# Performance work log

Measured on AMD Instinct MI355X. Metric: run time of the kernel, lower is better.

Reference implementation:

```python
import jax, jax.numpy as jnp
import numpy as np

N, E, G = 10000, 160000, 64
F, C1, C2, C3, K, NC = 128, 128, 256, 512, 5, 10


def setup_inputs() -> dict:
    key = jax.random.key(0)
    ks = jax.random.split(key, 12)
    s = 0.05
    return {
        "x": jax.random.normal(ks[0], (N, F), dtype=jnp.float32),
        "edge_index": jax.random.randint(ks[1], (2, E), 0, N, dtype=jnp.int64),
        "batch": jnp.sort(jax.random.randint(ks[2], (N,), 0, G, dtype=jnp.int64)),
        "W_cheb": jax.random.normal(ks[3], (K, F, C1), dtype=jnp.float32) * s,
        "b_cheb": jnp.zeros((C1,), jnp.float32),
        "W_g1": jax.random.normal(ks[4], (C1, C2), dtype=jnp.float32) * s,
        "b_g1": jnp.zeros((C2,), jnp.float32),
        "W_g2": jax.random.normal(ks[5], (C2, C3), dtype=jnp.float32) * s,
        "b_g2": jnp.zeros((C3,), jnp.float32),
        "w_gate": jax.random.normal(ks[6], (C3, 1), dtype=jnp.float32) * s,
        "b_gate": jnp.zeros((1,), jnp.float32),
        "W_fc": jax.random.normal(ks[7], (C3, NC), dtype=jnp.float32) * s,
        "b_fc": jnp.zeros((NC,), jnp.float32),
    }


def _deg_inv_sqrt(deg):
    return jnp.where(deg > 0, jax.lax.rsqrt(jnp.maximum(deg, 1e-12)), 0.0)


def cheb_conv(x, src, dst, W, b):
    # PyG ChebConv, sym normalization, lambda_max=2 => scaled Laplacian = -D^-1/2 A D^-1/2
    ones = jnp.ones((src.shape[0],), x.dtype)
    deg = jax.ops.segment_sum(ones, src, num_segments=N)
    dinv = _deg_inv_sqrt(deg)
    w = -(dinv[src] * dinv[dst])  # [E]

    def prop(h):
        return jax.ops.segment_sum(w[:, None] * h[src], dst, num_segments=N)

    tx0 = x
    tx1 = prop(x)
    out = tx0 @ W[0] + tx1 @ W[1]
    for k in range(2, W.shape[0]):
        tx2 = 2.0 * prop(tx1) - tx0
        out = out + tx2 @ W[k]
        tx0, tx1 = tx1, tx2
    return out + b


def gcn_conv(x, src, dst, W, b):
    # PyG GCNConv: add self-loops, sym norm D~^-1/2 (A+I) D~^-1/2, transform then aggregate
    loop = jnp.arange(N, dtype=src.dtype)
    src_a = jnp.concatenate([src, loop])
    dst_a = jnp.concatenate([dst, loop])
    ones = jnp.ones((src_a.shape[0],), x.dtype)
    deg = jax.ops.segment_sum(ones, dst_a, num_segments=N)
    dinv = _deg_inv_sqrt(deg)
    norm = dinv[src_a] * dinv[dst_a]  # [E+N]
    h = x @ W
    return jax.ops.segment_sum(norm[:, None] * h[src_a], dst_a, num_segments=N) + b


def attention_pool(x, batch, w_gate, b_gate):
    logits = (x @ w_gate + b_gate)[:, 0]  # [N]
    m = jax.ops.segment_max(logits, batch, num_segments=G)
    e = jnp.exp(logits - m[batch])
    s = jax.ops.segment_sum(e, batch, num_segments=G)
    alpha = e / s[batch]
    return jax.ops.segment_sum(alpha[:, None] * x, batch, num_segments=G)  # [G, C3]


def reference(x, edge_index, batch, W_cheb, b_cheb, W_g1, b_g1, W_g2, b_g2,
              w_gate, b_gate, W_fc, b_fc):
    src, dst = edge_index[0], edge_index[1]
    h = jax.nn.relu(cheb_conv(x, src, dst, W_cheb, b_cheb))
    h = jax.nn.relu(gcn_conv(h, src, dst, W_g1, b_g1))
    h = jax.nn.relu(gcn_conv(h, src, dst, W_g2, b_g2))
    g = attention_pool(h, batch, w_gate, b_gate)
    logits = g @ W_fc + b_fc
    return jax.nn.log_softmax(logits, axis=1)
```

## Files before the change

kernel.cpp:

```cpp
#include <hip/hip_runtime.h>
#include <hip/hip_bf16.h>
#include <math.h>

#define N_NODES 10000
#define N_EDGES 160000
#define N_GRAPHS 64
#define F_IN    128
#define C1_DIM  128
#define C2_DIM  256
#define C3_DIM  512
#define K_CHEB  5
#define NCLS    10
#define TC      (K_CHEB * F_IN)

typedef short v8s __attribute__((ext_vector_type(8)));
typedef float v4f __attribute__((ext_vector_type(4)));

static __device__ __forceinline__ unsigned short f2bf(float f) {
    unsigned u = __float_as_uint(f);
    unsigned r = (u + 0x7FFFu + ((u >> 16) & 1u)) >> 16;
    return (unsigned short)r;
}
static __device__ __forceinline__ float bf_lo(unsigned u) { return __uint_as_float(u << 16); }
static __device__ __forceinline__ float bf_hi(unsigned u) { return __uint_as_float(u & 0xFFFF0000u); }

#define PREP_A (N_NODES * 64)
#define PREP_B (TC * C1_DIM)
#define PREP_C (C1_DIM * C2_DIM)
#define PREP_D (C2_DIM * C3_DIM)
#define PREP_E N_NODES
#define PREP_F N_NODES
#define PREP_G N_EDGES
#define PREP_TOTAL (PREP_A + PREP_B + PREP_C + PREP_D + PREP_E + PREP_F + PREP_G)
__global__ void prep_kernel(const float* __restrict__ x, unsigned short* __restrict__ tcat,
                            const float* __restrict__ Wcheb, unsigned short* __restrict__ Wcb_t,
                            const float* __restrict__ Wg1, unsigned short* __restrict__ Wg1_t,
                            const float* __restrict__ Wg2, unsigned short* __restrict__ Wg2_t,
                            const int* __restrict__ batch, int* __restrict__ gptr,
                            float* __restrict__ logits,
                            const int* __restrict__ src, const int* __restrict__ dst,
                            int* __restrict__ cnt_s, int* __restrict__ cnt_d) {
    int id = blockIdx.x * blockDim.x + threadIdx.x;
    if (id < PREP_A) {
        int n = id >> 6, f = (id & 63) * 2;
        float2 v = *(const float2*)(x + (size_t)n * F_IN + f);
        ushort2 o; o.x = f2bf(v.x); o.y = f2bf(v.y);
        *(ushort2*)(tcat + (size_t)n * TC + f) = o;
        return;
    }
    id -= PREP_A;
    if (id < PREP_B) {
        int n = id % C1_DIM, k = id / C1_DIM;
        Wcb_t[(size_t)n * TC + k] = f2bf(Wcheb[(size_t)k * C1_DIM + n]);
        return;
    }
    id -= PREP_B;
    if (id < PREP_C) {
        int n = id % C2_DIM, k = id / C2_DIM;
        Wg1_t[(size_t)n * C1_DIM + k] = f2bf(Wg1[(size_t)k * C2_DIM + n]);
        return;
    }
    id -= PREP_C;
    if (id < PREP_D) {
        int n = id % C3_DIM, k = id / C3_DIM;
        Wg2_t[(size_t)n * C2_DIM + k] = f2bf(Wg2[(size_t)k * C3_DIM + n]);
        return;
    }
    id -= PREP_D;
    if (id < PREP_E) {
        int i = id;
        int b = batch[i];
        if (i == 0) { for (int g = 0; g <= b; g++) gptr[g] = 0; }
        else {
            int bp = batch[i - 1];
            for (int g = bp + 1; g <= b; g++) gptr[g] = i;
        }
        if (i == N_NODES - 1) { for (int g = b + 1; g <= N_GRAPHS; g++) gptr[g] = N_NODES; }
        return;
    }
    id -= PREP_E;
    if (id < PREP_F) { logits[id] = 0.0f; return; }
    id -= PREP_F;
    if (id < PREP_G) {
        atomicAdd(&cnt_s[src[id]], 1);
        atomicAdd(&cnt_d[dst[id]], 1);
    }
}

__global__ __launch_bounds__(256) void scan_kernel(const int* __restrict__ cnt_d,
                                                   int* __restrict__ rowptr, int n) {
    __shared__ int ldsc[N_NODES];
    __shared__ int sums[256];
    int tid = threadIdx.x;
    for (int i = tid; i < n; i += 256) ldsc[i] = cnt_d[i];
    __syncthreads();
    int chunk = (n + 255) / 256;
    int s0 = tid * chunk, s1 = min(n, s0 + chunk);
    if (s0 > n) s0 = n;
    int loc = 0;
    for (int i = s0; i < s1; i++) loc += ldsc[i];
    sums[tid] = loc;
    __syncthreads();
    for (int off = 1; off < 256; off <<= 1) {
        int t = (tid >= off) ? sums[tid - off] : 0;
        __syncthreads();
        sums[tid] += t;
        __syncthreads();
    }
    int pre = sums[tid] - loc;
    for (int i = s0; i < s1; i++) { int v = ldsc[i]; ldsc[i] = pre; pre += v; }
    __syncthreads();
    for (int i = tid; i < n; i += 256) rowptr[i] = ldsc[i];
    if (tid == 255) rowptr[n] = pre;
}

__global__ void fill_kernel(const int* __restrict__ src, const int* __restrict__ dst,
                            const int* __restrict__ cnt_s, const int* __restrict__ cnt_d,
                            const int* __restrict__ rowptr, int* __restrict__ fillc,
                            int* __restrict__ col, float* __restrict__ wch,
                            float* __restrict__ nrm, int E) {
    int e = blockIdx.x * blockDim.x + threadIdx.x;
    if (e >= E) return;
    int s = src[e], d = dst[e];
    int pos = rowptr[d] + atomicAdd(&fillc[d], 1);
    col[pos] = s;
    int cs = cnt_s[s], cd = cnt_s[d];
    float ds = (cs > 0) ? rsqrtf((float)cs) : 0.0f;
    float dd = (cd > 0) ? rsqrtf((float)cd) : 0.0f;
    wch[pos] = -(ds * dd);
    nrm[pos] = rsqrtf((float)cnt_d[s] + 1.0f) * rsqrtf((float)cnt_d[d] + 1.0f);
}

__global__ __launch_bounds__(256) void gather_cheb_bf(
        const unsigned short* __restrict__ tb, const int* __restrict__ rowptr,
        const int* __restrict__ col, const float* __restrict__ ew,
        const unsigned short* __restrict__ base, float alpha, float beta,
        unsigned short* __restrict__ outc, int n) {
    int w = (blockIdx.x * blockDim.x + threadIdx.x) >> 6;
    int lane = threadIdx.x & 63;
    if (w >= n) return;
    float a0 = 0.0f, a1 = 0.0f;
    int rs = rowptr[w], re = rowptr[w + 1];
    for (int b = rs; b < re; b += 64) {
        int cl = 0; float wl = 0.0f;
        if (b + lane < re) { cl = col[b + lane]; wl = ew[b + lane]; }
        int nk8 = (min(64, re - b) + 7) & ~7;
        for (int j = 0; j < nk8; j += 8) {
            int ss[8]; float ww[8]; unsigned uu[8];
            #pragma unroll
            for (int q = 0; q < 8; q++) { ss[q] = __shfl(cl, j + q); ww[q] = __shfl(wl, j + q); }
            #pragma unroll
            for (int q = 0; q < 8; q++) uu[q] = ((const unsigned*)(tb + (size_t)ss[q] * TC))[lane];
            #pragma unroll
            for (int q = 0; q < 8; q++) { a0 += ww[q] * bf_lo(uu[q]); a1 += ww[q] * bf_hi(uu[q]); }
        }
    }
    if (base) {
        unsigned ub = ((const unsigned*)(base + (size_t)w * TC))[lane];
        a0 = alpha * a0 + beta * bf_lo(ub);
        a1 = alpha * a1 + beta * bf_hi(ub);
    } else {
        a0 *= alpha; a1 *= alpha;
    }
    ushort2 o; o.x = f2bf(a0); o.y = f2bf(a1);
    *(ushort2*)(outc + (size_t)w * TC + lane * 2) = o;
}

template<int FPL>
__global__ __launch_bounds__(256) void gather_gcn_pre(
        const unsigned short* __restrict__ tb, const int* __restrict__ rowptr,
        const int* __restrict__ col, const float* __restrict__ ew,
        const int* __restrict__ cnt_d, unsigned short* __restrict__ z, int n) {
    const int C = FPL * 64;
    int w = (blockIdx.x * blockDim.x + threadIdx.x) >> 6;
    int lane = threadIdx.x & 63;
    if (w >= n) return;
    float acc[FPL];
    #pragma unroll
    for (int q = 0; q < FPL; q++) acc[q] = 0.0f;
    int rs = rowptr[w], re = rowptr[w + 1];
    for (int b = rs; b < re; b += 64) {
        int cl = 0; float wl = 0.0f;
        if (b + lane < re) { cl = col[b + lane]; wl = ew[b + lane]; }
        int nk8 = (min(64, re - b) + 7) & ~7;
        for (int j = 0; j < nk8; j += 8) {
            int ss[8]; float ww[8];
            #pragma unroll
            for (int q = 0; q < 8; q++) { ss[q] = __shfl(cl, j + q); ww[q] = __shfl(wl, j + q); }
            if constexpr (FPL == 2) {
                unsigned uu[8];
                #pragma unroll
                for (int q = 0; q < 8; q++) uu[q] = ((const unsigned*)(tb + (size_t)ss[q] * C))[lane];
                #pragma unroll
                for (int q = 0; q < 8; q++) {
                    acc[0] += ww[q] * bf_lo(uu[q]);
                    acc[1] += ww[q] * bf_hi(uu[q]);
                }
            } else {
                uint2 uu[8];
                #pragma unroll
                for (int q = 0; q < 8; q++) uu[q] = ((const uint2*)(tb + (size_t)ss[q] * C))[lane];
                #pragma unroll
                for (int q = 0; q < 8; q++) {
                    acc[0] += ww[q] * bf_lo(uu[q].x); acc[1] += ww[q] * bf_hi(uu[q].x);
                    acc[2] += ww[q] * bf_lo(uu[q].y); acc[3] += ww[q] * bf_hi(uu[q].y);
                }
            }
        }
    }
    float sn = 1.0f / (float)(cnt_d[w] + 1);
    if constexpr (FPL == 2) {
        unsigned u = ((const unsigned*)(tb + (size_t)w * C))[lane];
        acc[0] += sn * bf_lo(u); acc[1] += sn * bf_hi(u);
        ushort2 o; o.x = f2bf(acc[0]); o.y = f2bf(acc[1]);
        *(ushort2*)(z + (size_t)w * C + lane * 2) = o;
    } else {
        uint2 u = ((const uint2*)(tb + (size_t)w * C))[lane];
        acc[0] += sn * bf_lo(u.x); acc[1] += sn * bf_hi(u.x);
        acc[2] += sn * bf_lo(u.y); acc[3] += sn * bf_hi(u.y);
        ushort4 o; o.x = f2bf(acc[0]); o.y = f2bf(acc[1]);
        o.z = f2bf(acc[2]); o.w = f2bf(acc[3]);
        *(ushort4*)(z + (size_t)w * C + lane * 4) = o;
    }
}

template<int JT>
__global__ __launch_bounds__(256) void gemm_bf16(
        const unsigned short* __restrict__ A, const unsigned short* __restrict__ Bt,
        const float* __restrict__ bias, float* __restrict__ Cf,
        unsigned short* __restrict__ Cb, const float* __restrict__ wg,
        float* __restrict__ logits, int M, int K, int N, int relu) {
    int m0 = blockIdx.y * 64, n0 = blockIdx.x * (JT * 32);
    int wave = threadIdx.x >> 6, lane = threadIdx.x & 63;
    int wm = (wave & 1) * 32, wn = (wave >> 1) * (JT * 16);
    int l15 = lane & 15, quad = lane >> 4;

    v4f acc[2][JT];
    #pragma unroll
    for (int i = 0; i < 2; i++)
        #pragma unroll
        for (int j = 0; j < JT; j++) acc[i][j] = (v4f){0.f, 0.f, 0.f, 0.f};

    const unsigned short* Ab[2]; bool av[2];
    #pragma unroll
    for (int i = 0; i < 2; i++) {
        int row = m0 + wm + i * 16 + l15;
        av[i] = row < M;
        Ab[i] = A + (size_t)(av[i] ? row : 0) * K + quad * 8;
    }
    const unsigned short* Bb[JT];
    #pragma unroll
    for (int j = 0; j < JT; j++) {
        int coln = n0 + wn + j * 16 + l15;
        Bb[j] = Bt + (size_t)coln * K + quad * 8;
    }
    const v8s zero8 = {0, 0, 0, 0, 0, 0, 0, 0};

    for (int k0 = 0; k0 < K; k0 += 32) {
        v8s a[2], b[JT];
        #pragma unroll
        for (int i = 0; i < 2; i++) a[i] = av[i] ? *(const v8s*)(Ab[i] + k0) : zero8;
        #pragma unroll
        for (int j = 0; j < JT; j++) b[j] = *(const v8s*)(Bb[j] + k0);
        #pragma unroll
        for (int i = 0; i < 2; i++)
            #pragma unroll
            for (int j = 0; j < JT; j++)
                acc[i][j] = __builtin_amdgcn_mfma_f32_16x16x32_bf16(a[i], b[j], acc[i][j], 0, 0, 0);
    }

    float bv[JT], wgj[JT];
    #pragma unroll
    for (int j = 0; j < JT; j++) {
        int coln = n0 + wn + j * 16 + l15;
        bv[j] = bias[coln];
        wgj[j] = wg ? wg[coln] : 0.0f;
    }
    #pragma unroll
    for (int i = 0; i < 2; i++) {
        #pragma unroll
        for (int r = 0; r < 4; r++) {
            int row = m0 + wm + i * 16 + quad * 4 + r;
            if (row >= M) continue;
            float gval = 0.0f;
            #pragma unroll
            for (int j = 0; j < JT; j++) {
                int coln = n0 + wn + j * 16 + l15;
                float v = acc[i][j][r] + bv[j];
                if (relu) v = fmaxf(v, 0.0f);
                if (Cf) Cf[(size_t)row * N + coln] = v;
                else    Cb[(size_t)row * N + coln] = f2bf(v);
                gval += v * wgj[j];
            }
            if (wg) {
                #pragma unroll
                for (int off = 1; off < 16; off <<= 1) gval += __shfl_xor(gval, off);
                if (l15 == 0) atomicAdd(&logits[row], gval);
            }
        }
    }
}

__global__ __launch_bounds__(256) void pool_stats(float* __restrict__ logits,
                                                  const int* __restrict__ gptr,
                                                  float* __restrict__ pooled) {
    __shared__ float red[256];
    int g = blockIdx.x, tid = threadIdx.x;
    int gs = gptr[g], ge = gptr[g + 1];
    pooled[(size_t)g * C3_DIM + tid] = 0.0f;
    pooled[(size_t)g * C3_DIM + 256 + tid] = 0.0f;
    float m = -INFINITY;
    for (int i = gs + tid; i < ge; i += 256) m = fmaxf(m, logits[i]);
    red[tid] = m; __syncthreads();
    for (int off = 128; off > 0; off >>= 1) {
        if (tid < off) red[tid] = fmaxf(red[tid], red[tid + off]);
        __syncthreads();
    }
    m = red[0]; __syncthreads();
    float s = 0.0f;
    for (int i = gs + tid; i < ge; i += 256) s += expf(logits[i] - m);
    red[tid] = s; __syncthreads();
    for (int off = 128; off > 0; off >>= 1) {
        if (tid < off) red[tid] += red[tid + off];
        __syncthreads();
    }
    s = red[0];
    float sinv = (s > 0.0f) ? 1.0f / s : 0.0f;
    for (int i = gs + tid; i < ge; i += 256)
        logits[i] = expf(logits[i] - m) * sinv;
}

__global__ __launch_bounds__(256) void pool_partial(const unsigned short* __restrict__ h3b,
        const float* __restrict__ alpha, const int* __restrict__ gptr,
        float* __restrict__ pooled) {
    int g = blockIdx.x, sl = blockIdx.y, tid = threadIdx.x;
    int gs = gptr[g], ge = gptr[g + 1];
    int cnt = ge - gs;
    int i0 = gs + (cnt * sl) / 8;
    int i1 = gs + (cnt * (sl + 1)) / 8;
    float a0 = 0.0f, a1 = 0.0f;
    for (int i = i0; i < i1; i++) {
        float al = alpha[i];
        unsigned u = ((const unsigned*)(h3b + (size_t)i * C3_DIM))[tid];
        a0 += al * bf_lo(u);
        a1 += al * bf_hi(u);
    }
    if (i1 > i0) {
        atomicAdd(&pooled[(size_t)g * C3_DIM + tid * 2 + 0], a0);
        atomicAdd(&pooled[(size_t)g * C3_DIM + tid * 2 + 1], a1);
    }
}

__global__ void fc_kernel(const float* __restrict__ pooled, const float* __restrict__ Wfc,
                          const float* __restrict__ bfc, float* __restrict__ out) {
    int g = blockIdx.x;
    int t = threadIdx.x;
    float acc = -INFINITY;
    if (t < NCLS) {
        acc = bfc[t];
        for (int k = 0; k < C3_DIM; k++)
            acc += pooled[(size_t)g * C3_DIM + k] * Wfc[k * NCLS + t];
    }
    float m = acc;
    #pragma unroll
    for (int off = 8; off > 0; off >>= 1) m = fmaxf(m, __shfl_xor(m, off, 16));
    float e = (t < NCLS) ? expf(acc - m) : 0.0f;
    float s = e;
    #pragma unroll
    for (int off = 8; off > 0; off >>= 1) s += __shfl_xor(s, off, 16);
    if (t < NCLS) out[g * NCLS + t] = acc - m - logf(s);
}

extern "C" void kernel_launch(void* const* d_in, const int* in_sizes, int n_in,
                              void* d_out, int out_size, void* d_ws, size_t ws_size,
                              hipStream_t stream) {
    const float* x      = (const float*)d_in[0];
    const int*   ei     = (const int*)d_in[1];
    const int*   batch  = (const int*)d_in[2];
    const float* W_cheb = (const float*)d_in[3];
    const float* b_cheb = (const float*)d_in[4];
    const float* W_g1   = (const float*)d_in[5];
    const float* b_g1   = (const float*)d_in[6];
    const float* W_g2   = (const float*)d_in[7];
    const float* b_g2   = (const float*)d_in[8];
    const float* w_gate = (const float*)d_in[9];
    const float* W_fc   = (const float*)d_in[11];
    const float* b_fc   = (const float*)d_in[12];
    const int* src = ei;
    const int* dst = ei + N_EDGES;
    float* out = (float*)d_out;

    const int N = N_NODES, E = N_EDGES, G = N_GRAPHS;

    char* Wp = (char*)d_ws;
    auto alloc = [&](size_t bytes) {
        void* p = Wp;
        Wp += (bytes + 255) & ~(size_t)255;
        return p;
    };
    int*   cnt3    = (int*)alloc((size_t)3 * N * 4);
    int*   cnt_s   = cnt3;
    int*   cnt_d   = cnt3 + N;
    int*   fillc   = cnt3 + 2 * N;
    int*   rowptr  = (int*)alloc((N + 1) * 4);
    int*   col     = (int*)alloc(E * 4);
    float* wch     = (float*)alloc(E * 4);
    float* nrm     = (float*)alloc(E * 4);
    unsigned short* tcat  = (unsigned short*)alloc((size_t)N * TC * 2);
    unsigned short* h1b   = (unsigned short*)alloc((size_t)N * C1_DIM * 2);
    unsigned short* z1b   = (unsigned short*)alloc((size_t)N * C1_DIM * 2);
    unsigned short* h2b   = (unsigned short*)alloc((size_t)N * C2_DIM * 2);
    unsigned short* z2b   = (unsigned short*)alloc((size_t)N * C2_DIM * 2);
    unsigned short* h3b   = (unsigned short*)alloc((size_t)N * C3_DIM * 2);
    unsigned short* Wcb_t = (unsigned short*)alloc((size_t)TC * C1_DIM * 2);
    unsigned short* Wg1_t = (unsigned short*)alloc((size_t)C1_DIM * C2_DIM * 2);
    unsigned short* Wg2_t = (unsigned short*)alloc((size_t)C2_DIM * C3_DIM * 2);
    float* logits  = (float*)alloc(N * 4);
    int*   gptr    = (int*)alloc((G + 1) * 4);
    float* pooled  = (float*)alloc((size_t)G * C3_DIM * 4);

    dim3 blk(256);
    auto cdiv = [](int a, int b) { return (a + b - 1) / b; };

    hipMemsetAsync(cnt3, 0, (size_t)3 * N * sizeof(int), stream);
    hipLaunchKernelGGL(prep_kernel, dim3(cdiv(PREP_TOTAL, 256)), blk, 0, stream,
                       x, tcat, W_cheb, Wcb_t, W_g1, Wg1_t, W_g2, Wg2_t,
                       batch, gptr, logits, src, dst, cnt_s, cnt_d);

    hipLaunchKernelGGL(scan_kernel, dim3(1), blk, 0, stream, cnt_d, rowptr, N);
    hipLaunchKernelGGL(fill_kernel, dim3(cdiv(E, 256)), blk, 0, stream,
                       src, dst, cnt_s, cnt_d, rowptr, fillc, col, wch, nrm, E);

    const int NWB = cdiv(N, 4);

    hipLaunchKernelGGL(gather_cheb_bf, dim3(NWB), blk, 0, stream,
                       tcat + 0 * F_IN, rowptr, col, wch,
                       (const unsigned short*)nullptr, 1.0f, 0.0f, tcat + 1 * F_IN, N);
    hipLaunchKernelGGL(gather_cheb_bf, dim3(NWB), blk, 0, stream,
                       tcat + 1 * F_IN, rowptr, col, wch,
                       tcat + 0 * F_IN, 2.0f, -1.0f, tcat + 2 * F_IN, N);
    hipLaunchKernelGGL(gather_cheb_bf, dim3(NWB), blk, 0, stream,
                       tcat + 2 * F_IN, rowptr, col, wch,
                       tcat + 1 * F_IN, 2.0f, -1.0f, tcat + 3 * F_IN, N);
    hipLaunchKernelGGL(gather_cheb_bf, dim3(NWB), blk, 0, stream,
                       tcat + 3 * F_IN, rowptr, col, wch,
                       tcat + 2 * F_IN, 2.0f, -1.0f, tcat + 4 * F_IN, N);

    hipLaunchKernelGGL(gemm_bf16<2>, dim3(C1_DIM / 64, cdiv(N, 64)), blk, 0, stream,
                       tcat, Wcb_t, b_cheb, (float*)nullptr, h1b,
                       (const float*)nullptr, (float*)nullptr, N, TC, C1_DIM, 1);

    hipLaunchKernelGGL(gather_gcn_pre<2>, dim3(NWB), blk, 0, stream,
                       h1b, rowptr, col, nrm, cnt_d, z1b, N);
    hipLaunchKernelGGL(gemm_bf16<4>, dim3(C2_DIM / 128, cdiv(N, 64)), blk, 0, stream,
                       z1b, Wg1_t, b_g1, (float*)nullptr, h2b,
                       (const float*)nullptr, (float*)nullptr, N, C1_DIM, C2_DIM, 1);

    hipLaunchKernelGGL(gather_gcn_pre<4>, dim3(NWB), blk, 0, stream,
                       h2b, rowptr, col, nrm, cnt_d, z2b, N);
    hipLaunchKernelGGL(gemm_bf16<4>, dim3(C3_DIM / 128, cdiv(N, 64)), blk, 0, stream,
                       z2b, Wg2_t, b_g2, (float*)nullptr, h3b,
                       w_gate, logits, N, C2_DIM, C3_DIM, 1);

    hipLaunchKernelGGL(pool_stats, dim3(G), blk, 0, stream, logits, gptr, pooled);
    hipLaunchKernelGGL(pool_partial, dim3(G, 8), blk, 0, stream, h3b, logits, gptr, pooled);

    hipLaunchKernelGGL(fc_kernel, dim3(G), dim3(64), 0, stream, pooled, W_fc, b_fc, out);
}
```

Measured before the change: 265.4 us.

## Pack edge index and weight into int2, fuse pool stats, coalesce weight prep

Edge columns and weights are interleaved into int2 arrays, one for the Chebyshev weights and one for the GCN norms, so each gather kernel reads a single 8-byte load per edge instead of two separate arrays. The pool_stats kernel is merged into pool_partial: each block recomputes the per-graph max and sum and applies the softmax weight inline, and zeroing of the pooled buffer moves into prep_kernel. The weight-transpose loops in prep now index so consecutive threads write consecutive output elements. This saves a kernel launch and some memory traffic, at the cost of recomputing the segment statistics in all 8 slices of each graph.

After: 263.8 us. About the same (-0.6%).

```diff
diff --git a/kernel.cpp b/kernel.cpp
--- a/kernel.cpp
+++ b/kernel.cpp
@@ -30,14 +30,15 @@
 #define PREP_D (C2_DIM * C3_DIM)
 #define PREP_E N_NODES
 #define PREP_F N_NODES
+#define PREP_H (N_GRAPHS * C3_DIM)
 #define PREP_G N_EDGES
-#define PREP_TOTAL (PREP_A + PREP_B + PREP_C + PREP_D + PREP_E + PREP_F + PREP_G)
+#define PREP_TOTAL (PREP_A + PREP_B + PREP_C + PREP_D + PREP_E + PREP_F + PREP_H + PREP_G)
 __global__ void prep_kernel(const float* __restrict__ x, unsigned short* __restrict__ tcat,
                             const float* __restrict__ Wcheb, unsigned short* __restrict__ Wcb_t,
                             const float* __restrict__ Wg1, unsigned short* __restrict__ Wg1_t,
                             const float* __restrict__ Wg2, unsigned short* __restrict__ Wg2_t,
                             const int* __restrict__ batch, int* __restrict__ gptr,
-                            float* __restrict__ logits,
+                            float* __restrict__ logits, float* __restrict__ pooled,
                             const int* __restrict__ src, const int* __restrict__ dst,
                             int* __restrict__ cnt_s, int* __restrict__ cnt_d) {
     int id = blockIdx.x * blockDim.x + threadIdx.x;
@@ -50,19 +51,19 @@
     }
     id -= PREP_A;
     if (id < PREP_B) {
-        int n = id % C1_DIM, k = id / C1_DIM;
+        int k = id % TC, n = id / TC;
         Wcb_t[(size_t)n * TC + k] = f2bf(Wcheb[(size_t)k * C1_DIM + n]);
         return;
     }
     id -= PREP_B;
     if (id < PREP_C) {
-        int n = id % C2_DIM, k = id / C2_DIM;
+        int k = id % C1_DIM, n = id / C1_DIM;
         Wg1_t[(size_t)n * C1_DIM + k] = f2bf(Wg1[(size_t)k * C2_DIM + n]);
         return;
     }
     id -= PREP_C;
     if (id < PREP_D) {
-        int n = id % C3_DIM, k = id / C3_DIM;
+        int k = id % C2_DIM, n = id / C2_DIM;
         Wg2_t[(size_t)n * C2_DIM + k] = f2bf(Wg2[(size_t)k * C3_DIM + n]);
         return;
     }
@@ -81,6 +82,8 @@
     id -= PREP_E;
     if (id < PREP_F) { logits[id] = 0.0f; return; }
     id -= PREP_F;
+    if (id < PREP_H) { pooled[id] = 0.0f; return; }
+    id -= PREP_H;
     if (id < PREP_G) {
         atomicAdd(&cnt_s[src[id]], 1);
         atomicAdd(&cnt_d[dst[id]], 1);
@@ -117,23 +120,22 @@
 __global__ void fill_kernel(const int* __restrict__ src, const int* __restrict__ dst,
                             const int* __restrict__ cnt_s, const int* __restrict__ cnt_d,
                             const int* __restrict__ rowptr, int* __restrict__ fillc,
-                            int* __restrict__ col, float* __restrict__ wch,
-                            float* __restrict__ nrm, int E) {
+                            int2* __restrict__ ecb, int2* __restrict__ egc, int E) {
     int e = blockIdx.x * blockDim.x + threadIdx.x;
     if (e >= E) return;
     int s = src[e], d = dst[e];
     int pos = rowptr[d] + atomicAdd(&fillc[d], 1);
-    col[pos] = s;
     int cs = cnt_s[s], cd = cnt_s[d];
     float ds = (cs > 0) ? rsqrtf((float)cs) : 0.0f;
     float dd = (cd > 0) ? rsqrtf((float)cd) : 0.0f;
-    wch[pos] = -(ds * dd);
-    nrm[pos] = rsqrtf((float)cnt_d[s] + 1.0f) * rsqrtf((float)cnt_d[d] + 1.0f);
+    float nr = rsqrtf((float)cnt_d[s] + 1.0f) * rsqrtf((float)cnt_d[d] + 1.0f);
+    ecb[pos] = make_int2(s, __float_as_int(-(ds * dd)));
+    egc[pos] = make_int2(s, __float_as_int(nr));
 }
 
 __global__ __launch_bounds__(256) void gather_cheb_bf(
         const unsigned short* __restrict__ tb, const int* __restrict__ rowptr,
-        const int* __restrict__ col, const float* __restrict__ ew,
+        const int2* __restrict__ edges,
         const unsigned short* __restrict__ base, float alpha, float beta,
         unsigned short* __restrict__ outc, int n) {
     int w = (blockIdx.x * blockDim.x + threadIdx.x) >> 6;
@@ -143,7 +145,7 @@
     int rs = rowptr[w], re = rowptr[w + 1];
     for (int b = rs; b < re; b += 64) {
         int cl = 0; float wl = 0.0f;
-        if (b + lane < re) { cl = col[b + lane]; wl = ew[b + lane]; }
+        if (b + lane < re) { int2 e = edges[b + lane]; cl = e.x; wl = __int_as_float(e.y); }
         int nk8 = (min(64, re - b) + 7) & ~7;
         for (int j = 0; j < nk8; j += 8) {
             int ss[8]; float ww[8]; unsigned uu[8];
@@ -169,7 +171,7 @@
 template<int FPL>
 __global__ __launch_bounds__(256) void gather_gcn_pre(
         const unsigned short* __restrict__ tb, const int* __restrict__ rowptr,
-        const int* __restrict__ col, const float* __restrict__ ew,
+        const int2* __restrict__ edges,
         const int* __restrict__ cnt_d, unsigned short* __restrict__ z, int n) {
     const int C = FPL * 64;
     int w = (blockIdx.x * blockDim.x + threadIdx.x) >> 6;
@@ -181,7 +183,7 @@
     int rs = rowptr[w], re = rowptr[w + 1];
     for (int b = rs; b < re; b += 64) {
         int cl = 0; float wl = 0.0f;
-        if (b + lane < re) { cl = col[b + lane]; wl = ew[b + lane]; }
+        if (b + lane < re) { int2 e = edges[b + lane]; cl = e.x; wl = __int_as_float(e.y); }
         int nk8 = (min(64, re - b) + 7) & ~7;
         for (int j = 0; j < nk8; j += 8) {
             int ss[8]; float ww[8];
@@ -301,14 +303,12 @@
     }
 }
 
-__global__ __launch_bounds__(256) void pool_stats(float* __restrict__ logits,
-                                                  const int* __restrict__ gptr,
-                                                  float* __restrict__ pooled) {
+__global__ __launch_bounds__(256) void pool_partial(const unsigned short* __restrict__ h3b,
+        const float* __restrict__ logits, const int* __restrict__ gptr,
+        float* __restrict__ pooled) {
     __shared__ float red[256];
-    int g = blockIdx.x, tid = threadIdx.x;
+    int g = blockIdx.x, sl = blockIdx.y, tid = threadIdx.x;
     int gs = gptr[g], ge = gptr[g + 1];
-    pooled[(size_t)g * C3_DIM + tid] = 0.0f;
-    pooled[(size_t)g * C3_DIM + 256 + tid] = 0.0f;
     float m = -INFINITY;
     for (int i = gs + tid; i < ge; i += 256) m = fmaxf(m, logits[i]);
     red[tid] = m; __syncthreads();
@@ -326,21 +326,12 @@
     }
     s = red[0];
     float sinv = (s > 0.0f) ? 1.0f / s : 0.0f;
-    for (int i = gs + tid; i < ge; i += 256)
-        logits[i] = expf(logits[i] - m) * sinv;
-}
-
-__global__ __launch_bounds__(256) void pool_partial(const unsigned short* __restrict__ h3b,
-        const float* __restrict__ alpha, const int* __restrict__ gptr,
-        float* __restrict__ pooled) {
-    int g = blockIdx.x, sl = blockIdx.y, tid = threadIdx.x;
-    int gs = gptr[g], ge = gptr[g + 1];
     int cnt = ge - gs;
     int i0 = gs + (cnt * sl) / 8;
     int i1 = gs + (cnt * (sl + 1)) / 8;
     float a0 = 0.0f, a1 = 0.0f;
     for (int i = i0; i < i1; i++) {
-        float al = alpha[i];
+        float al = expf(logits[i] - m) * sinv;
         unsigned u = ((const unsigned*)(h3b + (size_t)i * C3_DIM))[tid];
         a0 += al * bf_lo(u);
         a1 += al * bf_hi(u);
@@ -403,9 +394,8 @@
     int*   cnt_d   = cnt3 + N;
     int*   fillc   = cnt3 + 2 * N;
     int*   rowptr  = (int*)alloc((N + 1) * 4);
-    int*   col     = (int*)alloc(E * 4);
-    float* wch     = (float*)alloc(E * 4);
-    float* nrm     = (float*)alloc(E * 4);
+    int2*  ecb     = (int2*)alloc((size_t)E * 8);
+    int2*  egc     = (int2*)alloc((size_t)E * 8);
     unsigned short* tcat  = (unsigned short*)alloc((size_t)N * TC * 2);
     unsigned short* h1b   = (unsigned short*)alloc((size_t)N * C1_DIM * 2);
     unsigned short* z1b   = (unsigned short*)alloc((size_t)N * C1_DIM * 2);
@@ -425,25 +415,25 @@
     hipMemsetAsync(cnt3, 0, (size_t)3 * N * sizeof(int), stream);
     hipLaunchKernelGGL(prep_kernel, dim3(cdiv(PREP_TOTAL, 256)), blk, 0, stream,
                        x, tcat, W_cheb, Wcb_t, W_g1, Wg1_t, W_g2, Wg2_t,
-                       batch, gptr, logits, src, dst, cnt_s, cnt_d);
+                       batch, gptr, logits, pooled, src, dst, cnt_s, cnt_d);
 
     hipLaunchKernelGGL(scan_kernel, dim3(1), blk, 0, stream, cnt_d, rowptr, N);
     hipLaunchKernelGGL(fill_kernel, dim3(cdiv(E, 256)), blk, 0, stream,
-                       src, dst, cnt_s, cnt_d, rowptr, fillc, col, wch, nrm, E);
+                       src, dst, cnt_s, cnt_d, rowptr, fillc, ecb, egc, E);
 
     const int NWB = cdiv(N, 4);
 
     hipLaunchKernelGGL(gather_cheb_bf, dim3(NWB), blk, 0, stream,
-                       tcat + 0 * F_IN, rowptr, col, wch,
+                       tcat + 0 * F_IN, rowptr, ecb,
                        (const unsigned short*)nullptr, 1.0f, 0.0f, tcat + 1 * F_IN, N);
     hipLaunchKernelGGL(gather_cheb_bf, dim3(NWB), blk, 0, stream,
-                       tcat + 1 * F_IN, rowptr, col, wch,
+                       tcat + 1 * F_IN, rowptr, ecb,
                        tcat + 0 * F_IN, 2.0f, -1.0f, tcat + 2 * F_IN, N);
     hipLaunchKernelGGL(gather_cheb_bf, dim3(NWB), blk, 0, stream,
-                       tcat + 2 * F_IN, rowptr, col, wch,
+                       tcat + 2 * F_IN, rowptr, ecb,
                        tcat + 1 * F_IN, 2.0f, -1.0f, tcat + 3 * F_IN, N);
     hipLaunchKernelGGL(gather_cheb_bf, dim3(NWB), blk, 0, stream,
-                       tcat + 3 * F_IN, rowptr, col, wch,
+                       tcat + 3 * F_IN, rowptr, ecb,
                        tcat + 2 * F_IN, 2.0f, -1.0f, tcat + 4 * F_IN, N);
 
     hipLaunchKernelGGL(gemm_bf16<2>, dim3(C1_DIM / 64, cdiv(N, 64)), blk, 0, stream,
@@ -451,19 +441,17 @@
                        (const float*)nullptr, (float*)nullptr, N, TC, C1_DIM, 1);
 
     hipLaunchKernelGGL(gather_gcn_pre<2>, dim3(NWB), blk, 0, stream,
-                       h1b, rowptr, col, nrm, cnt_d, z1b, N);
+                       h1b, rowptr, egc, cnt_d, z1b, N);
     hipLaunchKernelGGL(gemm_bf16<4>, dim3(C2_DIM / 128, cdiv(N, 64)), blk, 0, stream,
                        z1b, Wg1_t, b_g1, (float*)nullptr, h2b,
                        (const float*)nullptr, (float*)nullptr, N, C1_DIM, C2_DIM, 1);
 
     hipLaunchKernelGGL(gather_gcn_pre<4>, dim3(NWB), blk, 0, stream,
-                       h2b, rowptr, col, nrm, cnt_d, z2b, N);
+                       h2b, rowptr, egc, cnt_d, z2b, N);
     hipLaunchKernelGGL(gemm_bf16<4>, dim3(C3_DIM / 128, cdiv(N, 64)), blk, 0, stream,
                        z2b, Wg2_t, b_g2, (float*)nullptr, h3b,
                        w_gate, logits, N, C2_DIM, C3_DIM, 1);
 
-    hipLaunchKernelGGL(pool_stats, dim3(G), blk, 0, stream, logits, gptr, pooled);
     hipLaunchKernelGGL(pool_partial, dim3(G, 8), blk, 0, stream, h3b, logits, gptr, pooled);
-
     hipLaunchKernelGGL(fc_kernel, dim3(G), dim3(64), 0, stream, pooled, W_fc, b_fc, out);
 }
```
